# Kernel tuning notes

Measured on AMD Instinct MI355X. Metric: run time of the kernel, lower is better.

## Reference

```python
import jax, jax.numpy as jnp
import numpy as np
import math

D_MODEL = 1024
NUM_HEADS = 16
HEAD = D_MODEL // NUM_HEADS
EPS = 1e-5


def setup_inputs() -> dict:
    key = jax.random.key(0)
    ks = jax.random.split(key, 5)
    x = jax.random.normal(ks[0], (2, 2048, D_MODEL), dtype=jnp.float32)
    # parameters (torch.rand -> uniform [0,1) per the module; scaled here for numerics)
    wq = jax.random.uniform(ks[1], (NUM_HEADS, D_MODEL, HEAD), dtype=jnp.float32) * 0.02
    wk = jax.random.uniform(ks[2], (NUM_HEADS, D_MODEL, HEAD), dtype=jnp.float32) * 0.02
    wv = jax.random.uniform(ks[3], (NUM_HEADS, D_MODEL, HEAD), dtype=jnp.float32) * 0.02
    wo = jax.random.uniform(ks[4], (D_MODEL, D_MODEL), dtype=jnp.float32) * 0.02
    ln_w = jnp.ones((D_MODEL,), dtype=jnp.float32)
    ln_b = jnp.zeros((D_MODEL,), dtype=jnp.float32)
    return {"x": x, "ln_w": ln_w, "ln_b": ln_b, "wq": wq, "wk": wk, "wv": wv, "wo": wo}


def _layernorm(x, w, b):
    mean = jnp.mean(x, axis=-1, keepdims=True)
    var = jnp.var(x, axis=-1, keepdims=True)
    return (x - mean) * w / jnp.sqrt(var + EPS) + b


def reference(x, ln_w, ln_b, wq, wk, wv, wo):
    # pre-norm
    y = _layernorm(x, ln_w, ln_b)  # [b, s, d]
    seq_len = y.shape[-2]
    # per-head projections: [b, h, s, e]
    q = jnp.einsum('bsd,hde->bhse', y, wq)
    k = jnp.einsum('bsd,hde->bhse', y, wk)
    v = jnp.einsum('bsd,hde->bhse', y, wv)
    scores = jnp.einsum('bhse,bhte->bhst', q, k) / math.sqrt(HEAD)
    causal = jnp.triu(jnp.full((seq_len, seq_len), -jnp.inf, dtype=scores.dtype), k=1)
    scores = scores + causal
    weights = jax.nn.softmax(scores, axis=-1)
    attn = jnp.einsum('bhst,bhte->bshe', weights, v)  # merged transpose
    attn = attn.reshape(*attn.shape[:-2], -1)  # [b, s, d]
    out = attn @ wo
    return out + x
```

## Files before the change

kernel.cpp:

```cpp
#include <hip/hip_runtime.h>
#include <stdint.h>

typedef __bf16 bf16;
typedef __bf16 bf16x2 __attribute__((ext_vector_type(2)));
typedef __bf16 bf16x4 __attribute__((ext_vector_type(4)));
typedef __bf16 bf16x8 __attribute__((ext_vector_type(8)));
typedef float f32x4 __attribute__((ext_vector_type(4)));

#define D_MODEL 1024
#define NHEADS 16
#define HEADDIM 64
#define SEQ 2048
#define NBATCH 2

__device__ __forceinline__ void async_load16(const void* g, void* l) {
  __builtin_amdgcn_global_load_lds(
      (__attribute__((address_space(1))) void*)g,
      (__attribute__((address_space(3))) void*)l, 16, 0, 0);
}

__device__ __forceinline__ float fexp2(float x) {
#if __has_builtin(__builtin_amdgcn_exp2f)
  return __builtin_amdgcn_exp2f(x);
#else
  return exp2f(x);
#endif
}

__global__ __launch_bounds__(256)
void ln_and_transpose(const float* __restrict__ x, const float* __restrict__ lw,
                      const float* __restrict__ lb, bf16* __restrict__ y,
                      const float* __restrict__ wq, const float* __restrict__ wk,
                      const float* __restrict__ wv, const float* __restrict__ wo,
                      bf16* __restrict__ WqkvT, bf16* __restrict__ woT) {
  __shared__ float tile[64][65];
  __shared__ float ps[4], pq[4];
  int t = threadIdx.x;
  if (blockIdx.x < 4096) {
    int row = blockIdx.x;
    const float4 v = ((const float4*)(x + (size_t)row * D_MODEL))[t];
    float s = v.x + v.y + v.z + v.w;
    float sq = v.x * v.x + v.y * v.y + v.z * v.z + v.w * v.w;
#pragma unroll
    for (int d = 1; d < 64; d <<= 1) {
      s += __shfl_xor(s, d);
      sq += __shfl_xor(sq, d);
    }
    if ((t & 63) == 0) { ps[t >> 6] = s; pq[t >> 6] = sq; }
    __syncthreads();
    s = ps[0] + ps[1] + ps[2] + ps[3];
    sq = pq[0] + pq[1] + pq[2] + pq[3];
    float mean = s * (1.0f / D_MODEL);
    float var = sq * (1.0f / D_MODEL) - mean * mean;
    float rstd = rsqrtf(var + 1e-5f);
    float4 wv4 = ((const float4*)lw)[t];
    float4 bv = ((const float4*)lb)[t];
    bf16x4 o;
    o[0] = (bf16)((v.x - mean) * rstd * wv4.x + bv.x);
    o[1] = (bf16)((v.y - mean) * rstd * wv4.y + bv.y);
    o[2] = (bf16)((v.z - mean) * rstd * wv4.z + bv.z);
    o[3] = (bf16)((v.w - mean) * rstd * wv4.w + bv.w);
    ((bf16x4*)(y + (size_t)row * D_MODEL))[t] = o;
    return;
  }
  int blk = blockIdx.x - 4096;
  const float* s;
  bf16* d;
  int src_ld, dst_ld;
  if (blk < 768) {
    int wsel = blk >> 8;
    int rem = blk & 255;
    int h = rem >> 4, tr = rem & 15;
    const float* w3 = (wsel == 0) ? wq : (wsel == 1) ? wk : wv;
    s = w3 + (size_t)h * 65536 + (size_t)tr * 64 * 64;
    d = WqkvT + ((size_t)wsel << 20) + (size_t)h * 65536 + (size_t)tr * 64;
    src_ld = 64; dst_ld = 1024;
  } else {
    int r = blk - 768;
    int tr = r >> 4, tc = r & 15;
    s = wo + (size_t)(tr * 64) * 1024 + tc * 64;
    d = woT + (size_t)(tc * 64) * 1024 + tr * 64;
    src_ld = 1024; dst_ld = 1024;
  }
  int rr = t >> 4;
  int cc = (t & 15) << 2;
#pragma unroll
  for (int i = 0; i < 4; ++i) {
    float4 v = *(const float4*)&s[(size_t)(rr + i * 16) * src_ld + cc];
    tile[rr + i * 16][cc + 0] = v.x;
    tile[rr + i * 16][cc + 1] = v.y;
    tile[rr + i * 16][cc + 2] = v.z;
    tile[rr + i * 16][cc + 3] = v.w;
  }
  __syncthreads();
#pragma unroll
  for (int i = 0; i < 4; ++i) {
    int drow = rr + i * 16;
    bf16x4 o;
    o[0] = (bf16)tile[cc + 0][drow];
    o[1] = (bf16)tile[cc + 1][drow];
    o[2] = (bf16)tile[cc + 2][drow];
    o[3] = (bf16)tile[cc + 3][drow];
    *(bf16x4*)&d[(size_t)drow * dst_ld + cc] = o;
  }
}

template <int MODE, int BM, int BN>
__global__ __launch_bounds__(256)
void gemm_bt(const bf16* __restrict__ A, const bf16* __restrict__ Bt,
             int ntn, void* __restrict__ p0, void* __restrict__ p1,
             void* __restrict__ p2) {
  constexpr int NWR = BM / 64;
  constexpr int NWC = 4 / NWR;
  constexpr int NJ = BN / (16 * NWC);
  __shared__ __align__(16) bf16 As[2][BM * 64];
  __shared__ __align__(16) bf16 Bs[2][BN * 64];
  int cpx = gridDim.x >> 3;
  int wg = (blockIdx.x & 7) * cpx + (blockIdx.x >> 3);
  int bm = wg / ntn;
  int bn = wg % ntn;
  int t = threadIdx.x;
  int w = t >> 6, l = t & 63;
  int lg = l >> 4, lo = l & 15;
  int wr = w / NWC, wc = w % NWC;
  const bf16* Ab = A + (size_t)bm * BM * 1024;
  const bf16* Bb = Bt + (size_t)bn * BN * 1024;
  f32x4 acc[4][NJ];
#pragma unroll
  for (int i = 0; i < 4; ++i)
#pragma unroll
    for (int j = 0; j < NJ; ++j) acc[i][j] = (f32x4){0.f, 0.f, 0.f, 0.f};

  auto stage = [&](int bufi, int k0) {
#pragma unroll
    for (int it = 0; it < BM / 32; ++it) {
      int flat = it * 2048 + t * 8;
      int row = flat >> 6, sc = ((flat & 63) >> 3) ^ (row & 7);
      async_load16(Ab + (size_t)row * 1024 + k0 + sc * 8, &As[bufi][it * 2048 + w * 512]);
    }
#pragma unroll
    for (int it = 0; it < BN / 32; ++it) {
      int flat = it * 2048 + t * 8;
      int row = flat >> 6, sc = ((flat & 63) >> 3) ^ (row & 7);
      async_load16(Bb + (size_t)row * 1024 + k0 + sc * 8, &Bs[bufi][it * 2048 + w * 512]);
    }
  };

  stage(0, 0);
  __syncthreads();
  int buf = 0;
  for (int k0 = 0; k0 < 1024; k0 += 64) {
    if (k0 + 64 < 1024) stage(buf ^ 1, k0 + 64);
#pragma unroll
    for (int kk = 0; kk < 2; ++kk) {
      bf16x8 af[4], bfr[NJ];
#pragma unroll
      for (int i = 0; i < 4; ++i) {
        int row = wr * 64 + i * 16 + lo;
        af[i] = *(const bf16x8*)&As[buf][row * 64 + (((4 * kk + lg) ^ (lo & 7)) * 8)];
      }
#pragma unroll
      for (int j = 0; j < NJ; ++j) {
        int row = wc * (NJ * 16) + j * 16 + lo;
        bfr[j] = *(const bf16x8*)&Bs[buf][row * 64 + (((4 * kk + lg) ^ (lo & 7)) * 8)];
      }
#pragma unroll
      for (int i = 0; i < 4; ++i)
#pragma unroll
        for (int j = 0; j < NJ; ++j)
          acc[i][j] = __builtin_amdgcn_mfma_f32_16x16x32_bf16(af[i], bfr[j], acc[i][j], 0, 0, 0);
    }
    __syncthreads();
    buf ^= 1;
  }

  int mbase = bm * BM + wr * 64;
  int nbase = bn * BN + wc * (NJ * 16);
#pragma unroll
  for (int i = 0; i < 4; ++i) {
#pragma unroll
    for (int j = 0; j < NJ; ++j) {
      int row0 = mbase + i * 16 + lg * 4;
      int col = nbase + j * 16 + lo;
      if (MODE == 0) {
        if (col < 2048) {
          bf16* dst = (bf16*)(col < 1024 ? p0 : p1);
          int c = col & 1023;
          int h = c >> 6, e = c & 63;
#pragma unroll
          for (int r = 0; r < 4; ++r) {
            int row = row0 + r;
            dst[((((size_t)(row >> 11) * NHEADS + h) * SEQ) + (row & 2047)) * HEADDIM + e] =
                (bf16)acc[i][j][r];
          }
        } else {
          int c = col - 2048;
          int h = c >> 6, e = c & 63;
          int b_ = row0 >> 11, s_ = row0 & 2047;
          bf16x4 pk;
          pk[0] = (bf16)acc[i][j][0]; pk[1] = (bf16)acc[i][j][1];
          pk[2] = (bf16)acc[i][j][2]; pk[3] = (bf16)acc[i][j][3];
          *(bf16x4*)&((bf16*)p2)[(((size_t)b_ * NHEADS + h) * HEADDIM + e) * SEQ + s_] = pk;
        }
      } else {
#pragma unroll
        for (int r = 0; r < 4; ++r) {
          int row = row0 + r;
          float xr = ((const float*)p1)[(size_t)row * 1024 + col];
          ((float*)p0)[(size_t)row * 1024 + col] = acc[i][j][r] + xr;
        }
      }
    }
  }
}

__global__ __launch_bounds__(512)
void attn_kernel(const bf16* __restrict__ q, const bf16* __restrict__ k,
                 const bf16* __restrict__ vt, bf16* __restrict__ attn,
                 bf16* __restrict__ pO, float* __restrict__ plsum) {
  __shared__ __align__(16) bf16 Ks[2][64 * 64];
  __shared__ __align__(16) bf16 Vs[2][64 * 64];
  __shared__ __align__(16) bf16 P[8][16 * 64];
  const float C2 = 0.125f * 1.44269504f;
  const float MC = 128.0f * C2;
  int i = blockIdx.x;
  int slot = i >> 3;
  int bh = (i & 7) + 8 * (slot & 3);
  int ji = slot >> 2;
  int split, tb;
  if (ji < 8) { split = 0; tb = ji; }
  else { split = 1 + ((ji >> 4) & 1); tb = 15 - (ji & 7); }
  int c0 = (split == 2) ? tb + 1 : 0;
  int c1 = (split == 1) ? tb + 1 : 2 * tb + 2;
  int b = bh >> 4, h = bh & 15;
  int t = threadIdx.x, w = t >> 6, l = t & 63;
  int lg = l >> 4, lo = l & 15;
  const bf16* qp = q + (size_t)bh * SEQ * HEADDIM;
  const bf16* kp = k + (size_t)bh * SEQ * HEADDIM;
  const bf16* vp = vt + (size_t)bh * HEADDIM * SEQ;
  int q0 = tb * 128 + w * 16;
  int cd = q0 >> 6;
  int diag_rhs = (w & 3) * 16 + lo;

  bf16x8 qf0 = *(const bf16x8*)&qp[(size_t)(q0 + lo) * HEADDIM + 8 * lg];
  bf16x8 qf1 = *(const bf16x8*)&qp[(size_t)(q0 + lo) * HEADDIM + 32 + 8 * lg];

  auto stage = [&](int bufi, int kv0) {
    int row = t >> 3, c16 = t & 7;
    int sc = c16 ^ (row & 7);
    async_load16(kp + (size_t)(kv0 + row) * HEADDIM + sc * 8, &Ks[bufi][(t >> 6) * 512 + (t & 63) * 8]);
    async_load16(vp + (size_t)row * SEQ + kv0 + sc * 8, &Vs[bufi][(t >> 6) * 512 + (t & 63) * 8]);
  };

  f32x4 o[4];
#pragma unroll
  for (int nt = 0; nt < 4; ++nt) o[nt] = (f32x4){0.f, 0.f, 0.f, 0.f};
  float lsum = 0.f;

  int buf = 0;
  stage(0, c0 * 64);
  __syncthreads();

  for (int c = c0; c < c1; ++c) {
    if (c + 1 < c1) stage(buf ^ 1, (c + 1) * 64);

    if (c <= cd) {
      f32x4 s[4];
      __builtin_amdgcn_s_setprio(1);
#pragma unroll
      for (int nt = 0; nt < 4; ++nt) {
        s[nt] = (f32x4){0.f, 0.f, 0.f, 0.f};
        int krow = nt * 16 + lo;
        bf16x8 kf0 = *(const bf16x8*)&Ks[buf][krow * 64 + ((lg ^ (lo & 7)) * 8)];
        bf16x8 kf1 = *(const bf16x8*)&Ks[buf][krow * 64 + (((4 + lg) ^ (lo & 7)) * 8)];
        s[nt] = __builtin_amdgcn_mfma_f32_16x16x32_bf16(kf0, qf0, s[nt], 0, 0, 0);
        s[nt] = __builtin_amdgcn_mfma_f32_16x16x32_bf16(kf1, qf1, s[nt], 0, 0, 0);
      }
      __builtin_amdgcn_s_setprio(0);

      bf16x8 vf0[4], vf1[4];
#pragma unroll
      for (int nt = 0; nt < 4; ++nt) {
        int vrow = nt * 16 + lo;
        vf0[nt] = *(const bf16x8*)&Vs[buf][vrow * 64 + ((lg ^ (lo & 7)) * 8)];
        vf1[nt] = *(const bf16x8*)&Vs[buf][vrow * 64 + (((4 + lg) ^ (lo & 7)) * 8)];
      }

      if (c == cd) {
#pragma unroll
        for (int nt = 0; nt < 4; ++nt)
#pragma unroll
          for (int r = 0; r < 4; ++r)
            s[nt][r] = (16 * nt + 4 * lg + r <= diag_rhs) ? s[nt][r] : -1e30f;
      }

      float p[4][4];
      float psum[4];
#pragma unroll
      for (int nt = 0; nt < 4; ++nt) {
        psum[nt] = 0.f;
#pragma unroll
        for (int r = 0; r < 4; ++r) {
          float e = fexp2(fmaf(s[nt][r], C2, -MC));
          p[nt][r] = e;
          psum[nt] += e;
        }
      }
      float pst = (psum[0] + psum[1]) + (psum[2] + psum[3]);
      pst += __shfl_xor(pst, 16);
      pst += __shfl_xor(pst, 32);
      lsum += pst;

#pragma unroll
      for (int nt = 0; nt < 4; ++nt) {
        int chunk = (2 * nt + (lg >> 1)) ^ (lo & 7);
        int base = lo * 64 + chunk * 8 + 4 * (lg & 1);
        bf16x2 w0, w1;
        w0[0] = (bf16)p[nt][0]; w0[1] = (bf16)p[nt][1];
        w1[0] = (bf16)p[nt][2]; w1[1] = (bf16)p[nt][3];
        *(bf16x2*)&P[w][base] = w0;
        *(bf16x2*)&P[w][base + 2] = w1;
      }
      bf16x8 pf0 = *(const bf16x8*)&P[w][lo * 64 + ((lg ^ (lo & 7)) * 8)];
      bf16x8 pf1 = *(const bf16x8*)&P[w][lo * 64 + (((4 + lg) ^ (lo & 7)) * 8)];

      __builtin_amdgcn_s_setprio(1);
#pragma unroll
      for (int nt = 0; nt < 4; ++nt) {
        o[nt] = __builtin_amdgcn_mfma_f32_16x16x32_bf16(pf0, vf0[nt], o[nt], 0, 0, 0);
        o[nt] = __builtin_amdgcn_mfma_f32_16x16x32_bf16(pf1, vf1[nt], o[nt], 0, 0, 0);
      }
      __builtin_amdgcn_s_setprio(0);
    }

    __syncthreads();
    buf ^= 1;
  }

  if (split == 0) {
#pragma unroll
    for (int r = 0; r < 4; ++r) {
      float ls = __shfl(lsum, (l & 48) | (4 * lg + r));
      float inv = 1.0f / ls;
      int qrow = q0 + 4 * lg + r;
#pragma unroll
      for (int nt = 0; nt < 4; ++nt)
        attn[((size_t)b * SEQ + qrow) * D_MODEL + h * HEADDIM + nt * 16 + lo] =
            (bf16)(o[nt][r] * inv);
    }
  } else {
    int half = split - 1;
#pragma unroll
    for (int r = 0; r < 4; ++r) {
      float ls = __shfl(lsum, (l & 48) | (4 * lg + r));
      int prow = q0 - 1024 + 4 * lg + r;
      if (lo == 0) plsum[(half << 15) + (bh << 10) + prow] = ls;
      size_t base = (((size_t)half * 32 + bh) * 1024 + prow) * 64;
#pragma unroll
      for (int nt = 0; nt < 4; ++nt)
        pO[base + nt * 16 + lo] = (bf16)o[nt][r];
    }
  }
}

__global__ __launch_bounds__(256)
void merge_kernel(const bf16* __restrict__ pO, const float* __restrict__ plsum,
                  bf16* __restrict__ attn) {
  int tid = blockIdx.x * 256 + threadIdx.x;
  int bh = tid >> 14;
  int rem = tid & 16383;
  int srow = rem >> 4, q4 = rem & 15;
  int b = bh >> 4, h = bh & 15;
  float l = plsum[(bh << 10) + srow] + plsum[(1 << 15) + (bh << 10) + srow];
  float inv = 1.0f / l;
  size_t base = (((size_t)bh) * 1024 + srow) * 64 + q4 * 4;
  bf16x4 a1 = *(const bf16x4*)&pO[base];
  bf16x4 a2 = *(const bf16x4*)&pO[(size_t)32 * 1024 * 64 + base];
  bf16x4 o;
#pragma unroll
  for (int e = 0; e < 4; ++e)
    o[e] = (bf16)(((float)a1[e] + (float)a2[e]) * inv);
  *(bf16x4*)&attn[((size_t)b * SEQ + 1024 + srow) * D_MODEL + h * HEADDIM + q4 * 4] = o;
}

extern "C" void kernel_launch(void* const* d_in, const int* in_sizes, int n_in,
                              void* d_out, int out_size, void* d_ws, size_t ws_size,
                              hipStream_t stream) {
  const float* x = (const float*)d_in[0];
  const float* ln_w = (const float*)d_in[1];
  const float* ln_b = (const float*)d_in[2];
  const float* wq = (const float*)d_in[3];
  const float* wk = (const float*)d_in[4];
  const float* wv = (const float*)d_in[5];
  const float* wo = (const float*)d_in[6];
  float* out = (float*)d_out;
  char* ws = (char*)d_ws;

  bf16* y     = (bf16*)(ws);
  bf16* WqkvT = (bf16*)(ws + (8u << 20));
  bf16* woT   = (bf16*)(ws + (14u << 20));
  bf16* qb    = (bf16*)(ws + (16u << 20));
  bf16* kb    = (bf16*)(ws + (24u << 20));
  bf16* vtb   = (bf16*)(ws + (32u << 20));
  bf16* attnb = (bf16*)(ws + (40u << 20));
  bf16*  pO    = (bf16*)(ws);
  float* plsum = (float*)(ws + (8u << 20));

  ln_and_transpose<<<5120, 256, 0, stream>>>(x, ln_w, ln_b, y, wq, wk, wv, wo,
                                             WqkvT, woT);

  gemm_bt<0, 128, 192><<<512, 256, 0, stream>>>(y, WqkvT, 16, qb, kb, vtb);

  attn_kernel<<<dim3(768), 512, 0, stream>>>(qb, kb, vtb, attnb, pO, plsum);

  merge_kernel<<<2048, 256, 0, stream>>>(pO, plsum, attnb);

  gemm_bt<2, 64, 128><<<512, 256, 0, stream>>>(attnb, woT, 8, out, (void*)x, nullptr);
}
```

Baseline: 99.88 us.

## Give each attention wave two query tiles to reuse K/V fragments; vectorize merge

The attention kernel now runs 4 waves per block, each handling 32 query rows as two 16-row groups, so every K and V fragment read from LDS feeds twice as many MFMAs. Staging is reworked so 256 threads load the same 64x64 tiles in two passes, and causal masking and the output writes are adjusted per group. The merge kernel switches to 8-wide bf16 vectors with half the threads. In exchange, per-thread register use roughly doubles for accumulators and scores, and there are fewer waves per block to hide latency.

```diff
diff --git a/kernel.cpp b/kernel.cpp
--- a/kernel.cpp
+++ b/kernel.cpp
@@ -214,13 +214,13 @@
   }
 }
 
-__global__ __launch_bounds__(512)
+__global__ __launch_bounds__(256)
 void attn_kernel(const bf16* __restrict__ q, const bf16* __restrict__ k,
                  const bf16* __restrict__ vt, bf16* __restrict__ attn,
                  bf16* __restrict__ pO, float* __restrict__ plsum) {
   __shared__ __align__(16) bf16 Ks[2][64 * 64];
   __shared__ __align__(16) bf16 Vs[2][64 * 64];
-  __shared__ __align__(16) bf16 P[8][16 * 64];
+  __shared__ __align__(16) bf16 P[4][2][16 * 64];
   const float C2 = 0.125f * 1.44269504f;
   const float MC = 128.0f * C2;
   int i = blockIdx.x;
@@ -238,24 +238,35 @@
   const bf16* qp = q + (size_t)bh * SEQ * HEADDIM;
   const bf16* kp = k + (size_t)bh * SEQ * HEADDIM;
   const bf16* vp = vt + (size_t)bh * HEADDIM * SEQ;
-  int q0 = tb * 128 + w * 16;
+  int q0 = tb * 128 + w * 32;
   int cd = q0 >> 6;
-  int diag_rhs = (w & 3) * 16 + lo;
-
-  bf16x8 qf0 = *(const bf16x8*)&qp[(size_t)(q0 + lo) * HEADDIM + 8 * lg];
-  bf16x8 qf1 = *(const bf16x8*)&qp[(size_t)(q0 + lo) * HEADDIM + 32 + 8 * lg];
+
+  bf16x8 qf[2][2];
+#pragma unroll
+  for (int g = 0; g < 2; ++g) {
+    qf[g][0] = *(const bf16x8*)&qp[(size_t)(q0 + 16 * g + lo) * HEADDIM + 8 * lg];
+    qf[g][1] = *(const bf16x8*)&qp[(size_t)(q0 + 16 * g + lo) * HEADDIM + 32 + 8 * lg];
+  }
 
   auto stage = [&](int bufi, int kv0) {
-    int row = t >> 3, c16 = t & 7;
-    int sc = c16 ^ (row & 7);
-    async_load16(kp + (size_t)(kv0 + row) * HEADDIM + sc * 8, &Ks[bufi][(t >> 6) * 512 + (t & 63) * 8]);
-    async_load16(vp + (size_t)row * SEQ + kv0 + sc * 8, &Vs[bufi][(t >> 6) * 512 + (t & 63) * 8]);
+#pragma unroll
+    for (int it = 0; it < 2; ++it) {
+      int slot2 = it * 256 + w * 64 + l;
+      int row = slot2 >> 3, c16 = slot2 & 7;
+      int sc = c16 ^ (row & 7);
+      async_load16(kp + (size_t)(kv0 + row) * HEADDIM + sc * 8,
+                   &Ks[bufi][(it * 256 + w * 64) * 8]);
+      async_load16(vp + (size_t)row * SEQ + kv0 + sc * 8,
+                   &Vs[bufi][(it * 256 + w * 64) * 8]);
+    }
   };
 
-  f32x4 o[4];
-#pragma unroll
-  for (int nt = 0; nt < 4; ++nt) o[nt] = (f32x4){0.f, 0.f, 0.f, 0.f};
-  float lsum = 0.f;
+  f32x4 o[2][4];
+#pragma unroll
+  for (int g = 0; g < 2; ++g)
+#pragma unroll
+    for (int nt = 0; nt < 4; ++nt) o[g][nt] = (f32x4){0.f, 0.f, 0.f, 0.f};
+  float lsum[2] = {0.f, 0.f};
 
   int buf = 0;
   stage(0, c0 * 64);
@@ -265,16 +276,19 @@
     if (c + 1 < c1) stage(buf ^ 1, (c + 1) * 64);
 
     if (c <= cd) {
-      f32x4 s[4];
+      f32x4 s[2][4];
       __builtin_amdgcn_s_setprio(1);
 #pragma unroll
       for (int nt = 0; nt < 4; ++nt) {
-        s[nt] = (f32x4){0.f, 0.f, 0.f, 0.f};
         int krow = nt * 16 + lo;
         bf16x8 kf0 = *(const bf16x8*)&Ks[buf][krow * 64 + ((lg ^ (lo & 7)) * 8)];
         bf16x8 kf1 = *(const bf16x8*)&Ks[buf][krow * 64 + (((4 + lg) ^ (lo & 7)) * 8)];
-        s[nt] = __builtin_amdgcn_mfma_f32_16x16x32_bf16(kf0, qf0, s[nt], 0, 0, 0);
-        s[nt] = __builtin_amdgcn_mfma_f32_16x16x32_bf16(kf1, qf1, s[nt], 0, 0, 0);
+        s[0][nt] = (f32x4){0.f, 0.f, 0.f, 0.f};
+        s[1][nt] = (f32x4){0.f, 0.f, 0.f, 0.f};
+        s[0][nt] = __builtin_amdgcn_mfma_f32_16x16x32_bf16(kf0, qf[0][0], s[0][nt], 0, 0, 0);
+        s[1][nt] = __builtin_amdgcn_mfma_f32_16x16x32_bf16(kf0, qf[1][0], s[1][nt], 0, 0, 0);
+        s[0][nt] = __builtin_amdgcn_mfma_f32_16x16x32_bf16(kf1, qf[0][1], s[0][nt], 0, 0, 0);
+        s[1][nt] = __builtin_amdgcn_mfma_f32_16x16x32_bf16(kf1, qf[1][1], s[1][nt], 0, 0, 0);
       }
       __builtin_amdgcn_s_setprio(0);
 
@@ -288,47 +302,53 @@
 
       if (c == cd) {
 #pragma unroll
+        for (int g = 0; g < 2; ++g) {
+          int rhs = (w & 1) * 32 + 16 * g + lo;
+#pragma unroll
+          for (int nt = 0; nt < 4; ++nt)
+#pragma unroll
+            for (int r = 0; r < 4; ++r)
+              s[g][nt][r] = (16 * nt + 4 * lg + r <= rhs) ? s[g][nt][r] : -1e30f;
+        }
+      }
+
+#pragma unroll
+      for (int g = 0; g < 2; ++g) {
+        float psum = 0.f;
+#pragma unroll
         for (int nt = 0; nt < 4; ++nt)
 #pragma unroll
-          for (int r = 0; r < 4; ++r)
-            s[nt][r] = (16 * nt + 4 * lg + r <= diag_rhs) ? s[nt][r] : -1e30f;
-      }
-
-      float p[4][4];
-      float psum[4];
-#pragma unroll
-      for (int nt = 0; nt < 4; ++nt) {
-        psum[nt] = 0.f;
-#pragma unroll
-        for (int r = 0; r < 4; ++r) {
-          float e = fexp2(fmaf(s[nt][r], C2, -MC));
-          p[nt][r] = e;
-          psum[nt] += e;
+          for (int r = 0; r < 4; ++r) {
+            float e = fexp2(fmaf(s[g][nt][r], C2, -MC));
+            s[g][nt][r] = e;
+            psum += e;
+          }
+        psum += __shfl_xor(psum, 16);
+        psum += __shfl_xor(psum, 32);
+        lsum[g] += psum;
+
+#pragma unroll
+        for (int nt = 0; nt < 4; ++nt) {
+          int chunk = (2 * nt + (lg >> 1)) ^ (lo & 7);
+          int base = lo * 64 + chunk * 8 + 4 * (lg & 1);
+          bf16x2 w0, w1;
+          w0[0] = (bf16)s[g][nt][0]; w0[1] = (bf16)s[g][nt][1];
+          w1[0] = (bf16)s[g][nt][2]; w1[1] = (bf16)s[g][nt][3];
+          *(bf16x2*)&P[w][g][base] = w0;
+          *(bf16x2*)&P[w][g][base + 2] = w1;
         }
       }
-      float pst = (psum[0] + psum[1]) + (psum[2] + psum[3]);
-      pst += __shfl_xor(pst, 16);
-      pst += __shfl_xor(pst, 32);
-      lsum += pst;
-
-#pragma unroll
-      for (int nt = 0; nt < 4; ++nt) {
-        int chunk = (2 * nt + (lg >> 1)) ^ (lo & 7);
-        int base = lo * 64 + chunk * 8 + 4 * (lg & 1);
-        bf16x2 w0, w1;
-        w0[0] = (bf16)p[nt][0]; w0[1] = (bf16)p[nt][1];
-        w1[0] = (bf16)p[nt][2]; w1[1] = (bf16)p[nt][3];
-        *(bf16x2*)&P[w][base] = w0;
-        *(bf16x2*)&P[w][base + 2] = w1;
-      }
-      bf16x8 pf0 = *(const bf16x8*)&P[w][lo * 64 + ((lg ^ (lo & 7)) * 8)];
-      bf16x8 pf1 = *(const bf16x8*)&P[w][lo * 64 + (((4 + lg) ^ (lo & 7)) * 8)];
 
       __builtin_amdgcn_s_setprio(1);
 #pragma unroll
-      for (int nt = 0; nt < 4; ++nt) {
-        o[nt] = __builtin_amdgcn_mfma_f32_16x16x32_bf16(pf0, vf0[nt], o[nt], 0, 0, 0);
-        o[nt] = __builtin_amdgcn_mfma_f32_16x16x32_bf16(pf1, vf1[nt], o[nt], 0, 0, 0);
+      for (int g = 0; g < 2; ++g) {
+        bf16x8 pf0 = *(const bf16x8*)&P[w][g][lo * 64 + ((lg ^ (lo & 7)) * 8)];
+        bf16x8 pf1 = *(const bf16x8*)&P[w][g][lo * 64 + (((4 + lg) ^ (lo & 7)) * 8)];
+#pragma unroll
+        for (int nt = 0; nt < 4; ++nt) {
+          o[g][nt] = __builtin_amdgcn_mfma_f32_16x16x32_bf16(pf0, vf0[nt], o[g][nt], 0, 0, 0);
+          o[g][nt] = __builtin_amdgcn_mfma_f32_16x16x32_bf16(pf1, vf1[nt], o[g][nt], 0, 0, 0);
+        }
       }
       __builtin_amdgcn_s_setprio(0);
     }
@@ -339,27 +359,31 @@
 
   if (split == 0) {
 #pragma unroll
-    for (int r = 0; r < 4; ++r) {
-      float ls = __shfl(lsum, (l & 48) | (4 * lg + r));
-      float inv = 1.0f / ls;
-      int qrow = q0 + 4 * lg + r;
-#pragma unroll
-      for (int nt = 0; nt < 4; ++nt)
-        attn[((size_t)b * SEQ + qrow) * D_MODEL + h * HEADDIM + nt * 16 + lo] =
-            (bf16)(o[nt][r] * inv);
-    }
+    for (int g = 0; g < 2; ++g)
+#pragma unroll
+      for (int r = 0; r < 4; ++r) {
+        float ls = __shfl(lsum[g], (l & 48) | (4 * lg + r));
+        float inv = 1.0f / ls;
+        int qrow = q0 + 16 * g + 4 * lg + r;
+#pragma unroll
+        for (int nt = 0; nt < 4; ++nt)
+          attn[((size_t)b * SEQ + qrow) * D_MODEL + h * HEADDIM + nt * 16 + lo] =
+              (bf16)(o[g][nt][r] * inv);
+      }
   } else {
     int half = split - 1;
 #pragma unroll
-    for (int r = 0; r < 4; ++r) {
-      float ls = __shfl(lsum, (l & 48) | (4 * lg + r));
-      int prow = q0 - 1024 + 4 * lg + r;
-      if (lo == 0) plsum[(half << 15) + (bh << 10) + prow] = ls;
-      size_t base = (((size_t)half * 32 + bh) * 1024 + prow) * 64;
-#pragma unroll
-      for (int nt = 0; nt < 4; ++nt)
-        pO[base + nt * 16 + lo] = (bf16)o[nt][r];
-    }
+    for (int g = 0; g < 2; ++g)
+#pragma unroll
+      for (int r = 0; r < 4; ++r) {
+        float ls = __shfl(lsum[g], (l & 48) | (4 * lg + r));
+        int prow = q0 - 1024 + 16 * g + 4 * lg + r;
+        if (lo == 0) plsum[(half << 15) + (bh << 10) + prow] = ls;
+        size_t base = (((size_t)half * 32 + bh) * 1024 + prow) * 64;
+#pragma unroll
+        for (int nt = 0; nt < 4; ++nt)
+          pO[base + nt * 16 + lo] = (bf16)o[g][nt][r];
+      }
   }
 }
 
@@ -367,20 +391,20 @@
 void merge_kernel(const bf16* __restrict__ pO, const float* __restrict__ plsum,
                   bf16* __restrict__ attn) {
   int tid = blockIdx.x * 256 + threadIdx.x;
-  int bh = tid >> 14;
-  int rem = tid & 16383;
-  int srow = rem >> 4, q4 = rem & 15;
+  int bh = tid >> 13;
+  int rem = tid & 8191;
+  int srow = rem >> 3, q8 = rem & 7;
   int b = bh >> 4, h = bh & 15;
   float l = plsum[(bh << 10) + srow] + plsum[(1 << 15) + (bh << 10) + srow];
   float inv = 1.0f / l;
-  size_t base = (((size_t)bh) * 1024 + srow) * 64 + q4 * 4;
-  bf16x4 a1 = *(const bf16x4*)&pO[base];
-  bf16x4 a2 = *(const bf16x4*)&pO[(size_t)32 * 1024 * 64 + base];
-  bf16x4 o;
-#pragma unroll
-  for (int e = 0; e < 4; ++e)
+  size_t base = (((size_t)bh) * 1024 + srow) * 64 + q8 * 8;
+  bf16x8 a1 = *(const bf16x8*)&pO[base];
+  bf16x8 a2 = *(const bf16x8*)&pO[(size_t)32 * 1024 * 64 + base];
+  bf16x8 o;
+#pragma unroll
+  for (int e = 0; e < 8; ++e)
     o[e] = (bf16)(((float)a1[e] + (float)a2[e]) * inv);
-  *(bf16x4*)&attn[((size_t)b * SEQ + 1024 + srow) * D_MODEL + h * HEADDIM + q4 * 4] = o;
+  *(bf16x8*)&attn[((size_t)b * SEQ + 1024 + srow) * D_MODEL + h * HEADDIM + q8 * 8] = o;
 }
 
 extern "C" void kernel_launch(void* const* d_in, const int* in_sizes, int n_in,
@@ -411,9 +435,9 @@
 
   gemm_bt<0, 128, 192><<<512, 256, 0, stream>>>(y, WqkvT, 16, qb, kb, vtb);
 
-  attn_kernel<<<dim3(768), 512, 0, stream>>>(qb, kb, vtb, attnb, pO, plsum);
-
-  merge_kernel<<<2048, 256, 0, stream>>>(pO, plsum, attnb);
+  attn_kernel<<<dim3(768), 256, 0, stream>>>(qb, kb, vtb, attnb, pO, plsum);
+
+  merge_kernel<<<1024, 256, 0, stream>>>(pO, plsum, attnb);
 
   gemm_bt<2, 64, 128><<<512, 256, 0, stream>>>(attnb, woT, 8, out, (void*)x, nullptr);
 }
```

After: 107.0 us. 1.07x slower.
